# Kernel optimization log

Hardware: AMD Instinct MI355X
Metric: run time of the kernel (lower is better)

## Reference

```python
import jax, jax.numpy as jnp
import numpy as np

B, C, T = 4, 512, 2048
H = 8
GROUPS = 32


def setup_inputs() -> dict:
    key = jax.random.key(0)
    ks = jax.random.split(key, 7)
    x = jax.random.normal(ks[0], (B, C, T), dtype=jnp.float32)
    norm_w = jnp.ones((C,), dtype=jnp.float32)
    norm_b = jnp.zeros((C,), dtype=jnp.float32)
    # conv1d kernel-size-1 weights -> plain [out, in] matrices
    qkv_w = jax.random.normal(ks[1], (3 * C, C), dtype=jnp.float32) / np.sqrt(C)
    qkv_b = jnp.zeros((3 * C,), dtype=jnp.float32)
    proj_w = jax.random.normal(ks[2], (C, C), dtype=jnp.float32) / np.sqrt(C)
    proj_b = jnp.zeros((C,), dtype=jnp.float32)
    return {"x": x, "norm_w": norm_w, "norm_b": norm_b,
            "qkv_w": qkv_w, "qkv_b": qkv_b,
            "proj_w": proj_w, "proj_b": proj_b}


def _group_norm(x, w, b, groups=GROUPS, eps=1e-5):
    # x: [B, C, T]
    b_, c_, t_ = x.shape
    xg = x.reshape(b_, groups, c_ // groups, t_)
    mean = jnp.mean(xg, axis=(2, 3), keepdims=True)
    var = jnp.var(xg, axis=(2, 3), keepdims=True)
    xg = (xg - mean) * jax.lax.rsqrt(var + eps)
    xn = xg.reshape(b_, c_, t_)
    return xn * w[None, :, None] + b[None, :, None]


def reference(x, norm_w, norm_b, qkv_w, qkv_b, proj_w, proj_b):
    b, c, t = x.shape
    ch = c // H  # per-head channels
    scale = 1.0 / np.sqrt(np.sqrt(ch))

    xn = _group_norm(x, norm_w, norm_b)
    # 1x1 conv over T: [B, 3C, T]
    qkv = jnp.einsum('oc,bct->bot', qkv_w, xn) + qkv_b[None, :, None]
    q, k, v = jnp.split(qkv, 3, axis=1)               # each [B, C, T]
    q = q.reshape(b * H, ch, t)
    k = k.reshape(b * H, ch, t)
    v = v.reshape(b * H, ch, t)

    # full attention scores [B*H, T, T]
    weight = jnp.einsum('bct,bcs->bts', q * scale, k * scale)
    weight = jax.nn.softmax(weight.astype(jnp.float32), axis=-1).astype(weight.dtype)
    a = jnp.einsum('bts,bcs->bct', weight, v)          # [B*H, ch, T]
    h = a.reshape(b, c, t)

    h = jnp.einsum('oc,bct->bot', proj_w, h) + proj_b[None, :, None]
    return x + h
```

## Files before the change

kernel.cpp:

```cpp
#include <hip/hip_runtime.h>

#define NB 4
#define NC 512
#define NT 2048
#define NH 8
#define CHD 64
#define NG 32
#define GC 16
#define QK_SCALE 0.35355339059327373f
#define LOG2E 1.4426950408889634f

typedef __bf16 bf16_t;
typedef __bf16 bf16x8 __attribute__((ext_vector_type(8)));
typedef __bf16 bf16x4 __attribute__((ext_vector_type(4)));
typedef __bf16 bf16x2 __attribute__((ext_vector_type(2)));
typedef float f32x4 __attribute__((ext_vector_type(4)));
typedef float f32x16 __attribute__((ext_vector_type(16)));
typedef int i32x2 __attribute__((ext_vector_type(2)));
typedef unsigned int u32;

#if __has_builtin(__builtin_amdgcn_exp2f)
#define EXP2F(x) __builtin_amdgcn_exp2f(x)
#else
#define EXP2F(x) __exp2f(x)
#endif

__device__ __forceinline__ int probe_isbf(const void* norm_w) {
  return *(const unsigned*)norm_w == 0x3F803F80u;
}

__device__ __forceinline__ float load_sc(const void* p, int isbf, int i) {
  return isbf ? (float)((const bf16_t*)p)[i] : ((const float*)p)[i];
}

__device__ __forceinline__ u32 pk2bf(float a, float b) {
  union { bf16x2 h; u32 u; } c;
  c.h[0] = (bf16_t)a; c.h[1] = (bf16_t)b;
  return c.u;
}

__global__ __launch_bounds__(256) void sma_cvt_w(
    const void* __restrict__ Wqkv, const void* __restrict__ Wproj,
    const void* __restrict__ probe, bf16_t* __restrict__ wqb,
    bf16_t* __restrict__ wpb) {
  const int isbf = probe_isbf(probe);
  const size_t NQ = (size_t)3 * NC * NC;
  const size_t e = ((size_t)blockIdx.x * 256 + threadIdx.x) * 8;
  const void* src;
  bf16_t* dst;
  size_t off;
  if (e < NQ) { src = Wqkv; dst = wqb; off = e; }
  else        { src = Wproj; dst = wpb; off = e - NQ; }
  if (isbf) {
    *(bf16x8*)&dst[off] = *(const bf16x8*)&((const bf16_t*)src)[off];
  } else {
    const float* s = (const float*)src + off;
    const float4 a = *(const float4*)s;
    const float4 b2 = *(const float4*)(s + 4);
    bf16x8 o;
    o[0] = (bf16_t)a.x;  o[1] = (bf16_t)a.y;  o[2] = (bf16_t)a.z;  o[3] = (bf16_t)a.w;
    o[4] = (bf16_t)b2.x; o[5] = (bf16_t)b2.y; o[6] = (bf16_t)b2.z; o[7] = (bf16_t)b2.w;
    *(bf16x8*)&dst[off] = o;
  }
}

__global__ __launch_bounds__(256) void sma_gn_stats(
    const void* __restrict__ xv, const void* __restrict__ probe,
    float* __restrict__ partial) {
  const int isbf = probe_isbf(probe);
  const int blk = blockIdx.x;
  const size_t base = (size_t)blk * 8 * NT;

  float s = 0.f, ss = 0.f;
  if (isbf) {
    const bf16_t* xp = (const bf16_t*)xv + base;
    for (int i = threadIdx.x; i < 2048; i += 256) {
      bf16x8 v = *(const bf16x8*)&xp[(size_t)i * 8];
#pragma unroll
      for (int j = 0; j < 8; ++j) { float f = (float)v[j]; s += f; ss += f * f; }
    }
  } else {
    const float* xp = (const float*)xv + base;
    for (int i = threadIdx.x; i < 4096; i += 256) {
      float4 v = *(const float4*)&xp[(size_t)i * 4];
      s += v.x + v.y + v.z + v.w;
      ss += v.x * v.x + v.y * v.y + v.z * v.z + v.w * v.w;
    }
  }
#pragma unroll
  for (int m = 32; m; m >>= 1) { s += __shfl_xor(s, m); ss += __shfl_xor(ss, m); }
  __shared__ float red[2][4];
  const int wave = threadIdx.x >> 6, lane = threadIdx.x & 63;
  if (lane == 0) { red[0][wave] = s; red[1][wave] = ss; }
  __syncthreads();
  if (threadIdx.x == 0) {
    partial[blk * 2] = red[0][0] + red[0][1] + red[0][2] + red[0][3];
    partial[blk * 2 + 1] = red[1][0] + red[1][1] + red[1][2] + red[1][3];
  }
}

__global__ __launch_bounds__(256) void sma_gn_apply(
    const void* __restrict__ xv, const void* __restrict__ wv,
    const void* __restrict__ bv, const float* __restrict__ partial,
    bf16_t* __restrict__ xnT) {
  const int isbf = probe_isbf(wv);
  const int bb = blockIdx.x >> 6;
  const int tc = blockIdx.x & 63;
  const int t0 = tc * 32;
  const int tid = threadIdx.x;

  __shared__ float gs[NG][2];
  __shared__ float scsb[NC][2];
  __shared__ bf16_t XT[32][520];

  if (tid < NG) {
    const int p0 = (bb * 64 + tid * 2) * 2;
    const float s = partial[p0] + partial[p0 + 2];
    const float ss = partial[p0 + 1] + partial[p0 + 3];
    const float mean = s * (1.f / 32768.f);
    const float var = ss * (1.f / 32768.f) - mean * mean;
    gs[tid][0] = mean;
    gs[tid][1] = rsqrtf(var + 1e-5f);
  }
  __syncthreads();
  for (int c = tid; c < NC; c += 256) {
    const int g = c >> 4;
    const float sc = load_sc(wv, isbf, c) * gs[g][1];
    scsb[c][0] = sc;
    scsb[c][1] = load_sc(bv, isbf, c) - gs[g][0] * sc;
  }
  __syncthreads();

  if (isbf) {
    const bf16_t* xp = (const bf16_t*)xv + (size_t)bb * NC * NT;
#pragma unroll
    for (int i = 0; i < 8; ++i) {
      const int idx = tid + i * 256;
      const int c = idx >> 2, tv = idx & 3;
      bf16x8 v = *(const bf16x8*)&xp[(size_t)c * NT + t0 + tv * 8];
      const float sc = scsb[c][0], sb = scsb[c][1];
#pragma unroll
      for (int j = 0; j < 8; ++j) XT[tv * 8 + j][c] = (bf16_t)((float)v[j] * sc + sb);
    }
  } else {
    const float* xp = (const float*)xv + (size_t)bb * NC * NT;
#pragma unroll
    for (int i = 0; i < 16; ++i) {
      const int idx = tid + i * 256;
      const int c = idx >> 3, tv = idx & 7;
      float4 v = *(const float4*)&xp[(size_t)c * NT + t0 + tv * 4];
      const float sc = scsb[c][0], sb = scsb[c][1];
      XT[tv * 4 + 0][c] = (bf16_t)(v.x * sc + sb);
      XT[tv * 4 + 1][c] = (bf16_t)(v.y * sc + sb);
      XT[tv * 4 + 2][c] = (bf16_t)(v.z * sc + sb);
      XT[tv * 4 + 3][c] = (bf16_t)(v.w * sc + sb);
    }
  }
  __syncthreads();
  bf16_t* op = xnT + ((size_t)bb * NT + t0) * NC;
#pragma unroll
  for (int i = 0; i < 8; ++i) {
    const int idx = tid + i * 256;
    const int t = idx >> 6, cl = idx & 63;
    *(bf16x8*)&op[(size_t)t * NC + cl * 8] = *(const bf16x8*)&XT[t][cl * 8];
  }
}

__global__ __launch_bounds__(256) void sma_qkv_kernel(
    const bf16_t* __restrict__ W, const void* __restrict__ biasv,
    const void* __restrict__ probe, const bf16_t* __restrict__ xnT,
    bf16_t* __restrict__ qT, bf16_t* __restrict__ kT, bf16_t* __restrict__ vO) {
  const int isbf = probe_isbf(probe);
  const int nb = blockIdx.x;
  const int mb = blockIdx.y;
  const int tid = threadIdx.x;
  const int lane = tid & 63, wave = tid >> 6;
  const int l15 = lane & 15, quad = lane >> 4;
  const int wm = wave >> 1, wn = wave & 1;

  __shared__ bf16_t As[128][72];
  __shared__ bf16_t Bs[128][72];

  const int m0 = mb * 128, n0 = nb * 128;

  f32x4 acc[4][4];
#pragma unroll
  for (int i = 0; i < 4; ++i)
#pragma unroll
    for (int j = 0; j < 4; ++j) acc[i][j] = (f32x4){0.f, 0.f, 0.f, 0.f};

  bf16x8 ar[4], br[4];
#pragma unroll
  for (int it = 0; it < 4; ++it) {
    const int idx = tid + it * 256;
    const int row = idx >> 3, cv = idx & 7;
    ar[it] = *(const bf16x8*)&W[(size_t)(m0 + row) * NC + cv * 8];
    br[it] = *(const bf16x8*)&xnT[(size_t)(n0 + row) * NC + cv * 8];
  }

  for (int k0 = 0; k0 < NC; k0 += 64) {
    if (k0) __syncthreads();
#pragma unroll
    for (int it = 0; it < 4; ++it) {
      const int idx = tid + it * 256;
      const int row = idx >> 3, cv = idx & 7;
      *(bf16x8*)&As[row][cv * 8] = ar[it];
      *(bf16x8*)&Bs[row][cv * 8] = br[it];
    }
    __syncthreads();
    if (k0 + 64 < NC) {
      const int k1 = k0 + 64;
#pragma unroll
      for (int it = 0; it < 4; ++it) {
        const int idx = tid + it * 256;
        const int row = idx >> 3, cv = idx & 7;
        ar[it] = *(const bf16x8*)&W[(size_t)(m0 + row) * NC + k1 + cv * 8];
        br[it] = *(const bf16x8*)&xnT[(size_t)(n0 + row) * NC + k1 + cv * 8];
      }
    }
#pragma unroll
    for (int ks = 0; ks < 2; ++ks) {
      bf16x8 af[4], bfr[4];
#pragma unroll
      for (int mi = 0; mi < 4; ++mi)
        af[mi] = *(const bf16x8*)&As[wm * 64 + mi * 16 + l15][ks * 32 + quad * 8];
#pragma unroll
      for (int ni = 0; ni < 4; ++ni)
        bfr[ni] = *(const bf16x8*)&Bs[wn * 64 + ni * 16 + l15][ks * 32 + quad * 8];
#pragma unroll
      for (int mi = 0; mi < 4; ++mi)
#pragma unroll
        for (int ni = 0; ni < 4; ++ni)
          acc[mi][ni] = __builtin_amdgcn_mfma_f32_16x16x32_bf16(
              af[mi], bfr[ni], acc[mi][ni], 0, 0, 0);
    }
  }

  const int mw0 = m0 + wm * 64;
  const int bb = n0 >> 11;
  const int tbase = (n0 & 2047) + wn * 64;
  if (mw0 < 2 * NC) {
    bf16_t* dst = (mw0 < NC) ? qT : kT;
    const float scale = (mw0 < NC) ? (QK_SCALE * LOG2E) : QK_SCALE;
    const int h = (mw0 & (NC - 1)) >> 6;
#pragma unroll
    for (int mi = 0; mi < 4; ++mi) {
      const int ch0 = mi * 16 + quad * 4;
      float bs[4];
#pragma unroll
      for (int r = 0; r < 4; ++r) bs[r] = load_sc(biasv, isbf, mw0 + ch0 + r);
#pragma unroll
      for (int ni = 0; ni < 4; ++ni) {
        const int t = tbase + ni * 16 + l15;
        bf16x4 pk;
#pragma unroll
        for (int r = 0; r < 4; ++r)
          pk[r] = (bf16_t)((acc[mi][ni][r] + bs[r]) * scale);
        *(bf16x4*)&dst[((size_t)(bb * NH + h) * NT + t) * CHD + ch0] = pk;
      }
    }
  } else {
#pragma unroll
    for (int mi = 0; mi < 4; ++mi) {
#pragma unroll
      for (int r = 0; r < 4; ++r) {
        const int og = mw0 + mi * 16 + quad * 4 + r;
        const float bsc = load_sc(biasv, isbf, og);
        const int oc = og - 2 * NC;
#pragma unroll
        for (int ni = 0; ni < 4; ++ni) {
          const int t = tbase + ni * 16 + l15;
          vO[((size_t)bb * NC + oc) * NT + t] = (bf16_t)(acc[mi][ni][r] + bsc);
        }
      }
    }
  }
}

__global__ __launch_bounds__(512) void sma_attn_kernel(
    const bf16_t* __restrict__ qT, const bf16_t* __restrict__ kT,
    const bf16_t* __restrict__ vO, bf16_t* __restrict__ ht) {
  const int id = blockIdx.x;
  const int bh = id & 31, qt = id >> 5;
  const int b = bh >> 3, h = bh & 7;
  const int tid = threadIdx.x;
  const int lane = tid & 63, wave = tid >> 6;
  const int l31 = lane & 31, half = lane >> 5;

  const bf16_t* qb = qT + (size_t)bh * NT * CHD;
  const bf16_t* kb = kT + (size_t)bh * NT * CHD;
  const bf16_t* vb = vO + ((size_t)b * NC + h * CHD) * NT;

  __shared__ bf16_t Ks[64 * 64];
  __shared__ bf16_t Vs[64 * 64];
  __shared__ float lS[8][32];

  const int tq = qt * 256 + wave * 32 + l31;
  bf16x8 qf[4];
#pragma unroll
  for (int kc = 0; kc < 4; ++kc)
    qf[kc] = *(const bf16x8*)&qb[(size_t)tq * CHD + kc * 16 + half * 8];

  const int sR = tid >> 3;
  const int cvC = tid & 7;
  bf16x8 kr, vr;
  kr = *(const bf16x8*)&kb[(size_t)sR * CHD + cvC * 8];
  vr = *(const bf16x8*)&vb[(size_t)sR * NT + cvC * 8];

  f32x16 Oa[2];
#pragma unroll
  for (int i = 0; i < 2; ++i)
#pragma unroll
    for (int r = 0; r < 16; ++r) Oa[i][r] = 0.f;
  float lacc = 0.f;

  for (int st = 0; st < NT / 64; ++st) {
    __syncthreads();
    *(bf16x8*)&Ks[sR * 64 + ((cvC ^ (sR & 7)) * 8)] = kr;
    *(bf16x8*)&Vs[sR * 64 + ((cvC ^ (sR & 7)) * 8)] = vr;
    __syncthreads();
    if (st < NT / 64 - 1) {
      const int s0 = (st + 1) * 64;
      kr = *(const bf16x8*)&kb[(size_t)(s0 + sR) * CHD + cvC * 8];
      vr = *(const bf16x8*)&vb[(size_t)sR * NT + s0 + cvC * 8];
    }

    f32x16 sa[2];
#pragma unroll
    for (int i = 0; i < 2; ++i)
#pragma unroll
      for (int r = 0; r < 16; ++r) sa[i][r] = 0.f;
#pragma unroll
    for (int kc = 0; kc < 4; ++kc) {
#pragma unroll
      for (int sub = 0; sub < 2; ++sub) {
        const int srow = sub * 32 + l31;
        bf16x8 kf = *(const bf16x8*)&Ks[srow * 64 + (((kc * 2 + half) ^ (srow & 7)) * 8)];
        sa[sub] = __builtin_amdgcn_mfma_f32_32x32x16_bf16(kf, qf[kc], sa[sub], 0, 0, 0);
      }
    }

#pragma unroll
    for (int sub = 0; sub < 2; ++sub)
#pragma unroll
      for (int r = 0; r < 16; ++r) {
        const float p = EXP2F(sa[sub][r]);
        sa[sub][r] = p;
        lacc += p;
      }

    bf16x8 pfrag[4];
#pragma unroll
    for (int sub = 0; sub < 2; ++sub) {
#pragma unroll
      for (int kk = 0; kk < 2; ++kk) {
        const int b0 = kk * 8;
        const u32 E0 = pk2bf(sa[sub][b0 + 0], sa[sub][b0 + 1]);
        const u32 E1 = pk2bf(sa[sub][b0 + 2], sa[sub][b0 + 3]);
        const u32 O0 = pk2bf(sa[sub][b0 + 4], sa[sub][b0 + 5]);
        const u32 O1 = pk2bf(sa[sub][b0 + 6], sa[sub][b0 + 7]);
        const i32x2 sw0 = __builtin_amdgcn_permlane32_swap((int)E0, (int)O0, false, false);
        const i32x2 sw1 = __builtin_amdgcn_permlane32_swap((int)E1, (int)O1, false, false);
        union { u32 w[4]; bf16x8 v; } f;
        f.w[0] = (u32)sw0[0]; f.w[1] = (u32)sw1[0];
        f.w[2] = (u32)sw0[1]; f.w[3] = (u32)sw1[1];
        pfrag[sub * 2 + kk] = f.v;
      }
    }

#pragma unroll
    for (int ksp = 0; ksp < 4; ++ksp) {
#pragma unroll
      for (int sub = 0; sub < 2; ++sub) {
        const int crow = sub * 32 + l31;
        bf16x8 vf = *(const bf16x8*)&Vs[crow * 64 + (((ksp * 2 + half) ^ (crow & 7)) * 8)];
        Oa[sub] = __builtin_amdgcn_mfma_f32_32x32x16_bf16(pfrag[ksp], vf, Oa[sub], 0, 0, 0);
      }
    }
  }

  const float ltot = lacc + __shfl_xor(lacc, 32);
  if (half == 0) lS[wave][l31] = ltot;
  float invr[16];
#pragma unroll
  for (int rg = 0; rg < 4; ++rg) {
    const float4 l4 = *(const float4*)&lS[wave][rg * 8 + half * 4];
    invr[rg * 4 + 0] = 1.f / l4.x; invr[rg * 4 + 1] = 1.f / l4.y;
    invr[rg * 4 + 2] = 1.f / l4.z; invr[rg * 4 + 3] = 1.f / l4.w;
  }
#pragma unroll
  for (int sub = 0; sub < 2; ++sub) {
    const int c = h * CHD + sub * 32 + l31;
#pragma unroll
    for (int reg = 0; reg < 16; ++reg) {
      const int trow = (reg & 3) + 8 * (reg >> 2) + 4 * half;
      const int t = qt * 256 + wave * 32 + trow;
      ht[((size_t)b * NT + t) * NC + c] = (bf16_t)(Oa[sub][reg] * invr[reg]);
    }
  }
}

__global__ __launch_bounds__(256) void sma_proj_kernel(
    const bf16_t* __restrict__ W, const void* __restrict__ biasv,
    const void* __restrict__ probe, const bf16_t* __restrict__ ht,
    const void* __restrict__ xv, void* __restrict__ outv) {
  const int isbf = probe_isbf(probe);
  const int nb = blockIdx.x;
  const int mb = blockIdx.y;
  const int tid = threadIdx.x;
  const int lane = tid & 63, wave = tid >> 6;
  const int l15 = lane & 15, quad = lane >> 4;
  const int wm = wave >> 1, wn = wave & 1;

  __shared__ bf16_t As[64][72];
  __shared__ bf16_t Bs[128][72];

  const int m0 = mb * 64, n0 = nb * 128;

  f32x4 acc[2][4];
#pragma unroll
  for (int i = 0; i < 2; ++i)
#pragma unroll
    for (int j = 0; j < 4; ++j) acc[i][j] = (f32x4){0.f, 0.f, 0.f, 0.f};

  bf16x8 ar[2], br[4];
#pragma unroll
  for (int it = 0; it < 2; ++it) {
    const int idx = tid + it * 256;
    const int row = idx >> 3, cv = idx & 7;
    ar[it] = *(const bf16x8*)&W[(size_t)(m0 + row) * NC + cv * 8];
  }
#pragma unroll
  for (int it = 0; it < 4; ++it) {
    const int idx = tid + it * 256;
    const int row = idx >> 3, cv = idx & 7;
    br[it] = *(const bf16x8*)&ht[(size_t)(n0 + row) * NC + cv * 8];
  }

  for (int k0 = 0; k0 < NC; k0 += 64) {
    if (k0) __syncthreads();
#pragma unroll
    for (int it = 0; it < 2; ++it) {
      const int idx = tid + it * 256;
      const int row = idx >> 3, cv = idx & 7;
      *(bf16x8*)&As[row][cv * 8] = ar[it];
    }
#pragma unroll
    for (int it = 0; it < 4; ++it) {
      const int idx = tid + it * 256;
      const int row = idx >> 3, cv = idx & 7;
      *(bf16x8*)&Bs[row][cv * 8] = br[it];
    }
    __syncthreads();
    if (k0 + 64 < NC) {
      const int k1 = k0 + 64;
#pragma unroll
      for (int it = 0; it < 2; ++it) {
        const int idx = tid + it * 256;
        const int row = idx >> 3, cv = idx & 7;
        ar[it] = *(const bf16x8*)&W[(size_t)(m0 + row) * NC + k1 + cv * 8];
      }
#pragma unroll
      for (int it = 0; it < 4; ++it) {
        const int idx = tid + it * 256;
        const int row = idx >> 3, cv = idx & 7;
        br[it] = *(const bf16x8*)&ht[(size_t)(n0 + row) * NC + k1 + cv * 8];
      }
    }
#pragma unroll
    for (int ks = 0; ks < 2; ++ks) {
      bf16x8 af[2], bfr[4];
#pragma unroll
      for (int mi = 0; mi < 2; ++mi)
        af[mi] = *(const bf16x8*)&As[wm * 32 + mi * 16 + l15][ks * 32 + quad * 8];
#pragma unroll
      for (int ni = 0; ni < 4; ++ni)
        bfr[ni] = *(const bf16x8*)&Bs[wn * 64 + ni * 16 + l15][ks * 32 + quad * 8];
#pragma unroll
      for (int mi = 0; mi < 2; ++mi)
#pragma unroll
        for (int ni = 0; ni < 4; ++ni)
          acc[mi][ni] = __builtin_amdgcn_mfma_f32_16x16x32_bf16(
              af[mi], bfr[ni], acc[mi][ni], 0, 0, 0);
    }
  }

  const int bb = n0 >> 11;
  const int tbase = (n0 & 2047) + wn * 64;
  if (isbf) {
    const bf16_t* xb = (const bf16_t*)xv;
    bf16_t* op = (bf16_t*)outv;
#pragma unroll
    for (int mi = 0; mi < 2; ++mi)
#pragma unroll
      for (int r = 0; r < 4; ++r) {
        const int o = m0 + wm * 32 + mi * 16 + quad * 4 + r;
        const float bsc = load_sc(biasv, 1, o);
#pragma unroll
        for (int ni = 0; ni < 4; ++ni) {
          const int t = tbase + ni * 16 + l15;
          const size_t oi = ((size_t)bb * NC + o) * NT + t;
          op[oi] = (bf16_t)(acc[mi][ni][r] + bsc + (float)xb[oi]);
        }
      }
  } else {
    const float* xb = (const float*)xv;
    float* op = (float*)outv;
#pragma unroll
    for (int mi = 0; mi < 2; ++mi)
#pragma unroll
      for (int r = 0; r < 4; ++r) {
        const int o = m0 + wm * 32 + mi * 16 + quad * 4 + r;
        const float bsc = load_sc(biasv, 0, o);
#pragma unroll
        for (int ni = 0; ni < 4; ++ni) {
          const int t = tbase + ni * 16 + l15;
          const size_t oi = ((size_t)bb * NC + o) * NT + t;
          op[oi] = acc[mi][ni][r] + bsc + xb[oi];
        }
      }
  }
}

extern "C" void kernel_launch(void* const* d_in, const int* in_sizes, int n_in,
                              void* d_out, int out_size, void* d_ws, size_t ws_size,
                              hipStream_t stream) {
  const size_t NE = (size_t)NB * NC * NT;
  float* partial = (float*)d_ws;
  bf16_t* xnT = (bf16_t*)((char*)d_ws + 4096);
  bf16_t* qTp = xnT + NE;
  bf16_t* kTp = qTp + NE;
  bf16_t* vOp = kTp + NE;
  bf16_t* htp = vOp + NE;
  bf16_t* wqb = htp + NE;
  bf16_t* wpb = wqb + (size_t)3 * NC * NC;

  sma_cvt_w<<<dim3(512), 256, 0, stream>>>(d_in[3], d_in[5], d_in[1], wqb, wpb);
  sma_gn_stats<<<dim3(256), 256, 0, stream>>>(d_in[0], d_in[1], partial);
  sma_gn_apply<<<dim3(256), 256, 0, stream>>>(d_in[0], d_in[1], d_in[2], partial, xnT);
  sma_qkv_kernel<<<dim3(64, 12), 256, 0, stream>>>(
      wqb, d_in[4], d_in[1], xnT, qTp, kTp, vOp);
  sma_attn_kernel<<<dim3(256), 512, 0, stream>>>(qTp, kTp, vOp, htp);
  sma_proj_kernel<<<dim3(64, 8), 256, 0, stream>>>(
      wpb, d_in[6], d_in[1], htp, d_in[0], d_out);
}
```

Before: 163.1 us.

## Double-buffer K/V tiles in attention and halve query block size

The attention kernel now uses 256-thread blocks, each covering 128 queries, launched over 512 blocks instead of 256 blocks of 512 threads. K/V shared tiles are double-buffered, which removes one __syncthreads per iteration, and each thread stages two rows. The first QK MFMA now takes a zero accumulator instead of separately zeroing the score registers. The intent is more blocks per CU and fewer barriers, at the cost of twice as many K/V reloads from global/L2 across blocks and more shared memory per block.

```diff
diff --git a/kernel.cpp b/kernel.cpp
--- a/kernel.cpp
+++ b/kernel.cpp
@@ -277,7 +277,7 @@
   }
 }
 
-__global__ __launch_bounds__(512) void sma_attn_kernel(
+__global__ __launch_bounds__(256) void sma_attn_kernel(
     const bf16_t* __restrict__ qT, const bf16_t* __restrict__ kT,
     const bf16_t* __restrict__ vO, bf16_t* __restrict__ ht) {
   const int id = blockIdx.x;
@@ -291,11 +291,11 @@
   const bf16_t* kb = kT + (size_t)bh * NT * CHD;
   const bf16_t* vb = vO + ((size_t)b * NC + h * CHD) * NT;
 
-  __shared__ bf16_t Ks[64 * 64];
-  __shared__ bf16_t Vs[64 * 64];
-  __shared__ float lS[8][32];
-
-  const int tq = qt * 256 + wave * 32 + l31;
+  __shared__ bf16_t Ks[2][64 * 64];
+  __shared__ bf16_t Vs[2][64 * 64];
+  __shared__ float lS[4][32];
+
+  const int tq = qt * 128 + wave * 32 + l31;
   bf16x8 qf[4];
 #pragma unroll
   for (int kc = 0; kc < 4; ++kc)
@@ -303,39 +303,52 @@
 
   const int sR = tid >> 3;
   const int cvC = tid & 7;
-  bf16x8 kr, vr;
-  kr = *(const bf16x8*)&kb[(size_t)sR * CHD + cvC * 8];
-  vr = *(const bf16x8*)&vb[(size_t)sR * NT + cvC * 8];
+  const int swz = (cvC ^ (sR & 7)) * 8;
+  bf16x8 kr0, kr1, vr0, vr1;
+  kr0 = *(const bf16x8*)&kb[(size_t)sR * CHD + cvC * 8];
+  kr1 = *(const bf16x8*)&kb[(size_t)(sR + 32) * CHD + cvC * 8];
+  vr0 = *(const bf16x8*)&vb[(size_t)sR * NT + cvC * 8];
+  vr1 = *(const bf16x8*)&vb[(size_t)(sR + 32) * NT + cvC * 8];
 
   f32x16 Oa[2];
 #pragma unroll
   for (int i = 0; i < 2; ++i)
 #pragma unroll
     for (int r = 0; r < 16; ++r) Oa[i][r] = 0.f;
+  f32x16 z16;
+#pragma unroll
+  for (int r = 0; r < 16; ++r) z16[r] = 0.f;
   float lacc = 0.f;
 
   for (int st = 0; st < NT / 64; ++st) {
-    __syncthreads();
-    *(bf16x8*)&Ks[sR * 64 + ((cvC ^ (sR & 7)) * 8)] = kr;
-    *(bf16x8*)&Vs[sR * 64 + ((cvC ^ (sR & 7)) * 8)] = vr;
+    bf16_t* Kb = Ks[st & 1];
+    bf16_t* Vb = Vs[st & 1];
+    *(bf16x8*)&Kb[sR * 64 + swz] = kr0;
+    *(bf16x8*)&Kb[(sR + 32) * 64 + swz] = kr1;
+    *(bf16x8*)&Vb[sR * 64 + swz] = vr0;
+    *(bf16x8*)&Vb[(sR + 32) * 64 + swz] = vr1;
     __syncthreads();
     if (st < NT / 64 - 1) {
       const int s0 = (st + 1) * 64;
-      kr = *(const bf16x8*)&kb[(size_t)(s0 + sR) * CHD + cvC * 8];
-      vr = *(const bf16x8*)&vb[(size_t)sR * NT + s0 + cvC * 8];
+      kr0 = *(const bf16x8*)&kb[(size_t)(s0 + sR) * CHD + cvC * 8];
+      kr1 = *(const bf16x8*)&kb[(size_t)(s0 + sR + 32) * CHD + cvC * 8];
+      vr0 = *(const bf16x8*)&vb[(size_t)sR * NT + s0 + cvC * 8];
+      vr1 = *(const bf16x8*)&vb[(size_t)(sR + 32) * NT + s0 + cvC * 8];
     }
 
     f32x16 sa[2];
 #pragma unroll
-    for (int i = 0; i < 2; ++i)
-#pragma unroll
-      for (int r = 0; r < 16; ++r) sa[i][r] = 0.f;
-#pragma unroll
-    for (int kc = 0; kc < 4; ++kc) {
+    for (int sub = 0; sub < 2; ++sub) {
+      const int srow = sub * 32 + l31;
+      bf16x8 kf = *(const bf16x8*)&Kb[srow * 64 + ((half ^ (srow & 7)) * 8)];
+      sa[sub] = __builtin_amdgcn_mfma_f32_32x32x16_bf16(kf, qf[0], z16, 0, 0, 0);
+    }
+#pragma unroll
+    for (int kc = 1; kc < 4; ++kc) {
 #pragma unroll
       for (int sub = 0; sub < 2; ++sub) {
         const int srow = sub * 32 + l31;
-        bf16x8 kf = *(const bf16x8*)&Ks[srow * 64 + (((kc * 2 + half) ^ (srow & 7)) * 8)];
+        bf16x8 kf = *(const bf16x8*)&Kb[srow * 64 + (((kc * 2 + half) ^ (srow & 7)) * 8)];
         sa[sub] = __builtin_amdgcn_mfma_f32_32x32x16_bf16(kf, qf[kc], sa[sub], 0, 0, 0);
       }
     }
@@ -373,7 +386,7 @@
 #pragma unroll
       for (int sub = 0; sub < 2; ++sub) {
         const int crow = sub * 32 + l31;
-        bf16x8 vf = *(const bf16x8*)&Vs[crow * 64 + (((ksp * 2 + half) ^ (crow & 7)) * 8)];
+        bf16x8 vf = *(const bf16x8*)&Vb[crow * 64 + (((ksp * 2 + half) ^ (crow & 7)) * 8)];
         Oa[sub] = __builtin_amdgcn_mfma_f32_32x32x16_bf16(pfrag[ksp], vf, Oa[sub], 0, 0, 0);
       }
     }
@@ -394,7 +407,7 @@
 #pragma unroll
     for (int reg = 0; reg < 16; ++reg) {
       const int trow = (reg & 3) + 8 * (reg >> 2) + 4 * half;
-      const int t = qt * 256 + wave * 32 + trow;
+      const int t = qt * 128 + wave * 32 + trow;
       ht[((size_t)b * NT + t) * NC + c] = (bf16_t)(Oa[sub][reg] * invr[reg]);
     }
   }
@@ -540,7 +553,7 @@
   sma_gn_apply<<<dim3(256), 256, 0, stream>>>(d_in[0], d_in[1], d_in[2], partial, xnT);
   sma_qkv_kernel<<<dim3(64, 12), 256, 0, stream>>>(
       wqb, d_in[4], d_in[1], xnT, qTp, kTp, vOp);
-  sma_attn_kernel<<<dim3(256), 512, 0, stream>>>(qTp, kTp, vOp, htp);
+  sma_attn_kernel<<<dim3(512), 256, 0, stream>>>(qTp, kTp, vOp, htp);
   sma_proj_kernel<<<dim3(64, 8), 256, 0, stream>>>(
       wpb, d_in[6], d_in[1], htp, d_in[0], d_out);
 }
```

Result: slower. 173.9 us (+6.6%).

## Process two query strips per wave and double-buffer K/V tiles in attention

Applied to the files above, without the earlier changes.

Each wave now handles 64 query rows as two 32-row strips, so every K and V fragment read from LDS feeds twice as many MFMAs. The grid is halved to 128 blocks of 512 queries. K/V shared tiles are double-buffered, which removes one barrier per iteration. The trade-offs are higher register pressure from the doubled accumulators and only 128 blocks on a GPU with 256 CUs, which can leave half the machine idle.

```diff
diff --git a/kernel.cpp b/kernel.cpp
--- a/kernel.cpp
+++ b/kernel.cpp
@@ -277,7 +277,7 @@
   }
 }
 
-__global__ __launch_bounds__(512) void sma_attn_kernel(
+__global__ __launch_bounds__(512, 2) void sma_attn_kernel(
     const bf16_t* __restrict__ qT, const bf16_t* __restrict__ kT,
     const bf16_t* __restrict__ vO, bf16_t* __restrict__ ht) {
   const int id = blockIdx.x;
@@ -291,33 +291,43 @@
   const bf16_t* kb = kT + (size_t)bh * NT * CHD;
   const bf16_t* vb = vO + ((size_t)b * NC + h * CHD) * NT;
 
-  __shared__ bf16_t Ks[64 * 64];
-  __shared__ bf16_t Vs[64 * 64];
-  __shared__ float lS[8][32];
-
-  const int tq = qt * 256 + wave * 32 + l31;
-  bf16x8 qf[4];
-#pragma unroll
-  for (int kc = 0; kc < 4; ++kc)
-    qf[kc] = *(const bf16x8*)&qb[(size_t)tq * CHD + kc * 16 + half * 8];
+  __shared__ bf16_t Ks[2][64 * 64];
+  __shared__ bf16_t Vs[2][64 * 64];
+  __shared__ float lS[8][64];
+
+  const int tqb = qt * 512 + wave * 64;
+  bf16x8 qf[2][4];
+#pragma unroll
+  for (int strip = 0; strip < 2; ++strip)
+#pragma unroll
+    for (int kc = 0; kc < 4; ++kc)
+      qf[strip][kc] = *(const bf16x8*)
+          &qb[(size_t)(tqb + strip * 32 + l31) * CHD + kc * 16 + half * 8];
 
   const int sR = tid >> 3;
   const int cvC = tid & 7;
+  const int swz = (cvC ^ (sR & 7)) * 8;
   bf16x8 kr, vr;
   kr = *(const bf16x8*)&kb[(size_t)sR * CHD + cvC * 8];
   vr = *(const bf16x8*)&vb[(size_t)sR * NT + cvC * 8];
 
-  f32x16 Oa[2];
+  f32x16 Oa[2][2];
 #pragma unroll
   for (int i = 0; i < 2; ++i)
 #pragma unroll
-    for (int r = 0; r < 16; ++r) Oa[i][r] = 0.f;
-  float lacc = 0.f;
+    for (int j = 0; j < 2; ++j)
+#pragma unroll
+      for (int r = 0; r < 16; ++r) Oa[i][j][r] = 0.f;
+  f32x16 z16;
+#pragma unroll
+  for (int r = 0; r < 16; ++r) z16[r] = 0.f;
+  float lacc[2] = {0.f, 0.f};
 
   for (int st = 0; st < NT / 64; ++st) {
-    __syncthreads();
-    *(bf16x8*)&Ks[sR * 64 + ((cvC ^ (sR & 7)) * 8)] = kr;
-    *(bf16x8*)&Vs[sR * 64 + ((cvC ^ (sR & 7)) * 8)] = vr;
+    bf16_t* Kb = Ks[st & 1];
+    bf16_t* Vb = Vs[st & 1];
+    *(bf16x8*)&Kb[sR * 64 + swz] = kr;
+    *(bf16x8*)&Vb[sR * 64 + swz] = vr;
     __syncthreads();
     if (st < NT / 64 - 1) {
       const int s0 = (st + 1) * 64;
@@ -325,46 +335,56 @@
       vr = *(const bf16x8*)&vb[(size_t)sR * NT + s0 + cvC * 8];
     }
 
-    f32x16 sa[2];
-#pragma unroll
-    for (int i = 0; i < 2; ++i)
-#pragma unroll
-      for (int r = 0; r < 16; ++r) sa[i][r] = 0.f;
-#pragma unroll
-    for (int kc = 0; kc < 4; ++kc) {
+    bf16x8 kf[8];
+#pragma unroll
+    for (int kc = 0; kc < 4; ++kc)
 #pragma unroll
       for (int sub = 0; sub < 2; ++sub) {
         const int srow = sub * 32 + l31;
-        bf16x8 kf = *(const bf16x8*)&Ks[srow * 64 + (((kc * 2 + half) ^ (srow & 7)) * 8)];
-        sa[sub] = __builtin_amdgcn_mfma_f32_32x32x16_bf16(kf, qf[kc], sa[sub], 0, 0, 0);
-      }
-    }
-
-#pragma unroll
-    for (int sub = 0; sub < 2; ++sub)
-#pragma unroll
-      for (int r = 0; r < 16; ++r) {
-        const float p = EXP2F(sa[sub][r]);
-        sa[sub][r] = p;
-        lacc += p;
-      }
-
-    bf16x8 pfrag[4];
-#pragma unroll
-    for (int sub = 0; sub < 2; ++sub) {
-#pragma unroll
-      for (int kk = 0; kk < 2; ++kk) {
-        const int b0 = kk * 8;
-        const u32 E0 = pk2bf(sa[sub][b0 + 0], sa[sub][b0 + 1]);
-        const u32 E1 = pk2bf(sa[sub][b0 + 2], sa[sub][b0 + 3]);
-        const u32 O0 = pk2bf(sa[sub][b0 + 4], sa[sub][b0 + 5]);
-        const u32 O1 = pk2bf(sa[sub][b0 + 6], sa[sub][b0 + 7]);
-        const i32x2 sw0 = __builtin_amdgcn_permlane32_swap((int)E0, (int)O0, false, false);
-        const i32x2 sw1 = __builtin_amdgcn_permlane32_swap((int)E1, (int)O1, false, false);
-        union { u32 w[4]; bf16x8 v; } f;
-        f.w[0] = (u32)sw0[0]; f.w[1] = (u32)sw1[0];
-        f.w[2] = (u32)sw0[1]; f.w[3] = (u32)sw1[1];
-        pfrag[sub * 2 + kk] = f.v;
+        kf[kc * 2 + sub] =
+            *(const bf16x8*)&Kb[srow * 64 + (((kc * 2 + half) ^ (srow & 7)) * 8)];
+      }
+
+    bf16x8 pfrag[2][4];
+#pragma unroll
+    for (int strip = 0; strip < 2; ++strip) {
+      f32x16 sa[2];
+#pragma unroll
+      for (int sub = 0; sub < 2; ++sub)
+        sa[sub] = __builtin_amdgcn_mfma_f32_32x32x16_bf16(
+            kf[sub], qf[strip][0], z16, 0, 0, 0);
+#pragma unroll
+      for (int kc = 1; kc < 4; ++kc)
+#pragma unroll
+        for (int sub = 0; sub < 2; ++sub)
+          sa[sub] = __builtin_amdgcn_mfma_f32_32x32x16_bf16(
+              kf[kc * 2 + sub], qf[strip][kc], sa[sub], 0, 0, 0);
+
+#pragma unroll
+      for (int sub = 0; sub < 2; ++sub)
+#pragma unroll
+        for (int r = 0; r < 16; ++r) {
+          const float p = EXP2F(sa[sub][r]);
+          sa[sub][r] = p;
+          lacc[strip] += p;
+        }
+
+#pragma unroll
+      for (int sub = 0; sub < 2; ++sub) {
+#pragma unroll
+        for (int kk = 0; kk < 2; ++kk) {
+          const int b0 = kk * 8;
+          const u32 E0 = pk2bf(sa[sub][b0 + 0], sa[sub][b0 + 1]);
+          const u32 E1 = pk2bf(sa[sub][b0 + 2], sa[sub][b0 + 3]);
+          const u32 O0 = pk2bf(sa[sub][b0 + 4], sa[sub][b0 + 5]);
+          const u32 O1 = pk2bf(sa[sub][b0 + 6], sa[sub][b0 + 7]);
+          const i32x2 sw0 = __builtin_amdgcn_permlane32_swap((int)E0, (int)O0, false, false);
+          const i32x2 sw1 = __builtin_amdgcn_permlane32_swap((int)E1, (int)O1, false, false);
+          union { u32 w[4]; bf16x8 v; } f;
+          f.w[0] = (u32)sw0[0]; f.w[1] = (u32)sw1[0];
+          f.w[2] = (u32)sw0[1]; f.w[3] = (u32)sw1[1];
+          pfrag[strip][sub * 2 + kk] = f.v;
+        }
       }
     }
 
@@ -373,29 +393,38 @@
 #pragma unroll
       for (int sub = 0; sub < 2; ++sub) {
         const int crow = sub * 32 + l31;
-        bf16x8 vf = *(const bf16x8*)&Vs[crow * 64 + (((ksp * 2 + half) ^ (crow & 7)) * 8)];
-        Oa[sub] = __builtin_amdgcn_mfma_f32_32x32x16_bf16(pfrag[ksp], vf, Oa[sub], 0, 0, 0);
-      }
-    }
-  }
-
-  const float ltot = lacc + __shfl_xor(lacc, 32);
-  if (half == 0) lS[wave][l31] = ltot;
-  float invr[16];
-#pragma unroll
-  for (int rg = 0; rg < 4; ++rg) {
-    const float4 l4 = *(const float4*)&lS[wave][rg * 8 + half * 4];
-    invr[rg * 4 + 0] = 1.f / l4.x; invr[rg * 4 + 1] = 1.f / l4.y;
-    invr[rg * 4 + 2] = 1.f / l4.z; invr[rg * 4 + 3] = 1.f / l4.w;
-  }
-#pragma unroll
-  for (int sub = 0; sub < 2; ++sub) {
-    const int c = h * CHD + sub * 32 + l31;
-#pragma unroll
-    for (int reg = 0; reg < 16; ++reg) {
-      const int trow = (reg & 3) + 8 * (reg >> 2) + 4 * half;
-      const int t = qt * 256 + wave * 32 + trow;
-      ht[((size_t)b * NT + t) * NC + c] = (bf16_t)(Oa[sub][reg] * invr[reg]);
+        bf16x8 vf = *(const bf16x8*)&Vb[crow * 64 + (((ksp * 2 + half) ^ (crow & 7)) * 8)];
+        Oa[0][sub] = __builtin_amdgcn_mfma_f32_32x32x16_bf16(
+            pfrag[0][ksp], vf, Oa[0][sub], 0, 0, 0);
+        Oa[1][sub] = __builtin_amdgcn_mfma_f32_32x32x16_bf16(
+            pfrag[1][ksp], vf, Oa[1][sub], 0, 0, 0);
+      }
+    }
+  }
+
+#pragma unroll
+  for (int strip = 0; strip < 2; ++strip) {
+    const float ltot = lacc[strip] + __shfl_xor(lacc[strip], 32);
+    if (half == 0) lS[wave][strip * 32 + l31] = ltot;
+  }
+#pragma unroll
+  for (int strip = 0; strip < 2; ++strip) {
+    float invr[16];
+#pragma unroll
+    for (int rg = 0; rg < 4; ++rg) {
+      const float4 l4 = *(const float4*)&lS[wave][strip * 32 + rg * 8 + half * 4];
+      invr[rg * 4 + 0] = 1.f / l4.x; invr[rg * 4 + 1] = 1.f / l4.y;
+      invr[rg * 4 + 2] = 1.f / l4.z; invr[rg * 4 + 3] = 1.f / l4.w;
+    }
+#pragma unroll
+    for (int sub = 0; sub < 2; ++sub) {
+      const int c = h * CHD + sub * 32 + l31;
+#pragma unroll
+      for (int reg = 0; reg < 16; ++reg) {
+        const int trow = (reg & 3) + 8 * (reg >> 2) + 4 * half;
+        const int t = tqb + strip * 32 + trow;
+        ht[((size_t)b * NT + t) * NC + c] = (bf16_t)(Oa[strip][sub][reg] * invr[reg]);
+      }
     }
   }
 }
@@ -540,7 +569,7 @@
   sma_gn_apply<<<dim3(256), 256, 0, stream>>>(d_in[0], d_in[1], d_in[2], partial, xnT);
   sma_qkv_kernel<<<dim3(64, 12), 256, 0, stream>>>(
       wqb, d_in[4], d_in[1], xnT, qTp, kTp, vOp);
-  sma_attn_kernel<<<dim3(256), 512, 0, stream>>>(qTp, kTp, vOp, htp);
+  sma_attn_kernel<<<dim3(128), 512, 0, stream>>>(qTp, kTp, vOp, htp);
   sma_proj_kernel<<<dim3(64, 8), 256, 0, stream>>>(
       wpb, d_in[6], d_in[1], htp, d_in[0], d_out);
 }
```

Measured after the change: 185.6 us. 13.8% more time.

## Software-pipeline attention loop with triple-buffered LDS and deferred PV MFMA

Applied to the files above, without the earlier changes.

Triple-buffers the K/V shared-memory tiles so each iteration needs only one barrier instead of two. The P·V MFMA for the previous tile is deferred into the next iteration, right after the current QK MFMAs, so matrix work overlaps the exp/pack phase across waves. It also raises wave priority around the MFMA blocks. In exchange it uses three times the LDS for K/V and keeps pfrag live across iterations, which adds register pressure and may reduce occupancy.

```diff
diff --git a/kernel.cpp b/kernel.cpp
--- a/kernel.cpp
+++ b/kernel.cpp
@@ -291,8 +291,8 @@
   const bf16_t* kb = kT + (size_t)bh * NT * CHD;
   const bf16_t* vb = vO + ((size_t)b * NC + h * CHD) * NT;
 
-  __shared__ bf16_t Ks[64 * 64];
-  __shared__ bf16_t Vs[64 * 64];
+  __shared__ bf16_t Ks[3][64 * 64];
+  __shared__ bf16_t Vs[3][64 * 64];
   __shared__ float lS[8][32];
 
   const int tq = qt * 256 + wave * 32 + l31;
@@ -303,6 +303,7 @@
 
   const int sR = tid >> 3;
   const int cvC = tid & 7;
+  const int swz = (cvC ^ (sR & 7)) * 8;
   bf16x8 kr, vr;
   kr = *(const bf16x8*)&kb[(size_t)sR * CHD + cvC * 8];
   vr = *(const bf16x8*)&vb[(size_t)sR * NT + cvC * 8];
@@ -312,33 +313,58 @@
   for (int i = 0; i < 2; ++i)
 #pragma unroll
     for (int r = 0; r < 16; ++r) Oa[i][r] = 0.f;
+  f32x16 z16;
+#pragma unroll
+  for (int r = 0; r < 16; ++r) z16[r] = 0.f;
   float lacc = 0.f;
 
-  for (int st = 0; st < NT / 64; ++st) {
+  bf16x8 pfrag[4];
+  const int NS = NT / 64;
+  int bi = 0, pbi = 2;
+
+  for (int st = 0; st < NS; ++st) {
+    bf16_t* Kb = Ks[bi];
+    bf16_t* Vb = Vs[bi];
+    *(bf16x8*)&Kb[sR * 64 + swz] = kr;
+    *(bf16x8*)&Vb[sR * 64 + swz] = vr;
     __syncthreads();
-    *(bf16x8*)&Ks[sR * 64 + ((cvC ^ (sR & 7)) * 8)] = kr;
-    *(bf16x8*)&Vs[sR * 64 + ((cvC ^ (sR & 7)) * 8)] = vr;
-    __syncthreads();
-    if (st < NT / 64 - 1) {
+    if (st < NS - 1) {
       const int s0 = (st + 1) * 64;
       kr = *(const bf16x8*)&kb[(size_t)(s0 + sR) * CHD + cvC * 8];
       vr = *(const bf16x8*)&vb[(size_t)sR * NT + s0 + cvC * 8];
     }
 
     f32x16 sa[2];
-#pragma unroll
-    for (int i = 0; i < 2; ++i)
-#pragma unroll
-      for (int r = 0; r < 16; ++r) sa[i][r] = 0.f;
-#pragma unroll
-    for (int kc = 0; kc < 4; ++kc) {
+    __builtin_amdgcn_s_setprio(1);
+#pragma unroll
+    for (int sub = 0; sub < 2; ++sub) {
+      const int srow = sub * 32 + l31;
+      bf16x8 kf = *(const bf16x8*)&Kb[srow * 64 + ((half ^ (srow & 7)) * 8)];
+      sa[sub] = __builtin_amdgcn_mfma_f32_32x32x16_bf16(kf, qf[0], z16, 0, 0, 0);
+    }
+#pragma unroll
+    for (int kc = 1; kc < 4; ++kc) {
 #pragma unroll
       for (int sub = 0; sub < 2; ++sub) {
         const int srow = sub * 32 + l31;
-        bf16x8 kf = *(const bf16x8*)&Ks[srow * 64 + (((kc * 2 + half) ^ (srow & 7)) * 8)];
+        bf16x8 kf = *(const bf16x8*)&Kb[srow * 64 + (((kc * 2 + half) ^ (srow & 7)) * 8)];
         sa[sub] = __builtin_amdgcn_mfma_f32_32x32x16_bf16(kf, qf[kc], sa[sub], 0, 0, 0);
       }
     }
+
+    if (st) {
+      bf16_t* Vp = Vs[pbi];
+#pragma unroll
+      for (int ksp = 0; ksp < 4; ++ksp) {
+#pragma unroll
+        for (int sub = 0; sub < 2; ++sub) {
+          const int crow = sub * 32 + l31;
+          bf16x8 vf = *(const bf16x8*)&Vp[crow * 64 + (((ksp * 2 + half) ^ (crow & 7)) * 8)];
+          Oa[sub] = __builtin_amdgcn_mfma_f32_32x32x16_bf16(pfrag[ksp], vf, Oa[sub], 0, 0, 0);
+        }
+      }
+    }
+    __builtin_amdgcn_s_setprio(0);
 
 #pragma unroll
     for (int sub = 0; sub < 2; ++sub)
@@ -348,8 +374,6 @@
         sa[sub][r] = p;
         lacc += p;
       }
-
-    bf16x8 pfrag[4];
 #pragma unroll
     for (int sub = 0; sub < 2; ++sub) {
 #pragma unroll
@@ -368,15 +392,23 @@
       }
     }
 
+    pbi = bi;
+    bi = (bi == 2) ? 0 : bi + 1;
+  }
+
+  {
+    bf16_t* Vp = Vs[pbi];
+    __builtin_amdgcn_s_setprio(1);
 #pragma unroll
     for (int ksp = 0; ksp < 4; ++ksp) {
 #pragma unroll
       for (int sub = 0; sub < 2; ++sub) {
         const int crow = sub * 32 + l31;
-        bf16x8 vf = *(const bf16x8*)&Vs[crow * 64 + (((ksp * 2 + half) ^ (crow & 7)) * 8)];
+        bf16x8 vf = *(const bf16x8*)&Vp[crow * 64 + (((ksp * 2 + half) ^ (crow & 7)) * 8)];
         Oa[sub] = __builtin_amdgcn_mfma_f32_32x32x16_bf16(pfrag[ksp], vf, Oa[sub], 0, 0, 0);
       }
     }
+    __builtin_amdgcn_s_setprio(0);
   }
 
   const float ltot = lacc + __shfl_xor(lacc, 32);
```

Result: no change. 163.6 us (+0.3%).
